# Kernel tuning notes

Measured on AMD Instinct MI355X. Metric: run time of the kernel, lower is better.

The kernel has to match this reference:

```python
import jax, jax.numpy as jnp
import numpy as np

N, E, G = 30000, 240000, 1500
EMB, NODE_DIM, EDGE_DIM, TASKS = 300, 9, 3, 12
L_ENC, L_RAT = 5, 2
GAMMA, T_CON = 0.4, 0.2


def _w(key, shape, fan_in):
    return jax.random.normal(key, shape, jnp.float32) / np.float32(np.sqrt(fan_in))


def setup_inputs() -> dict:
    key = jax.random.key(0)
    ks = jax.random.split(key, 32)
    inp = {}
    inp['x'] = jax.random.normal(ks[0], (N, NODE_DIM), jnp.float32)
    inp['edge_attr'] = jax.random.normal(ks[1], (E, EDGE_DIM), jnp.float32)
    inp['edge_index'] = jax.random.randint(ks[2], (2, E), 0, N, jnp.int32)
    b = jnp.sort(jax.random.randint(ks[3], (N,), 0, G, jnp.int32))
    inp['batch'] = b.at[0].set(0).at[-1].set(G - 1)
    u = jax.random.uniform(ks[4], (N, 2), jnp.float32, 1e-6, 1.0 - 1e-6)
    inp['gumbel'] = -jnp.log(-jnp.log(u))  # standard Gumbel noise (tau=1)
    inp['perm'] = jax.random.permutation(ks[5], G).astype(jnp.int32)
    inp['W_enc'] = _w(ks[6], (NODE_DIM, EMB), NODE_DIM)
    inp['b_enc'] = jnp.zeros((EMB,), jnp.float32)
    inp['We_g'] = _w(ks[7], (L_ENC, EDGE_DIM, EMB), EDGE_DIM)
    inp['be_g'] = jnp.zeros((L_ENC, EMB), jnp.float32)
    inp['W1_g'] = _w(ks[8], (L_ENC, EMB, 2 * EMB), EMB)
    inp['b1_g'] = jnp.zeros((L_ENC, 2 * EMB), jnp.float32)
    inp['W2_g'] = _w(ks[9], (L_ENC, 2 * EMB, EMB), 2 * EMB)
    inp['b2_g'] = jnp.zeros((L_ENC, EMB), jnp.float32)
    inp['We_r'] = _w(ks[10], (L_RAT, EDGE_DIM, EMB), EDGE_DIM)
    inp['be_r'] = jnp.zeros((L_RAT, EMB), jnp.float32)
    inp['W1_r'] = _w(ks[11], (L_RAT, EMB, 2 * EMB), EMB)
    inp['b1_r'] = jnp.zeros((L_RAT, 2 * EMB), jnp.float32)
    inp['W2_r'] = _w(ks[12], (L_RAT, 2 * EMB, EMB), 2 * EMB)
    inp['b2_r'] = jnp.zeros((L_RAT, EMB), jnp.float32)
    inp['Wg1'] = _w(ks[13], (EMB, 2 * EMB), EMB)
    inp['bg1'] = jnp.zeros((2 * EMB,), jnp.float32)
    inp['Wg2'] = _w(ks[14], (2 * EMB, 2), 2 * EMB)
    inp['bg2'] = jnp.zeros((2,), jnp.float32)
    inp['Wp1'] = _w(ks[15], (EMB, 2 * EMB), EMB)
    inp['bp1'] = jnp.zeros((2 * EMB,), jnp.float32)
    inp['Wp2'] = _w(ks[16], (2 * EMB, TASKS), 2 * EMB)
    inp['bp2'] = jnp.zeros((TASKS,), jnp.float32)
    return inp


def _gin_stack(x, src, dst, edge_attr, We, be, W1, b1, W2, b2):
    # GIN-style message passing with edge features, residual, JK='last'.
    L = We.shape[0]
    for l in range(L):
        e = edge_attr @ We[l] + be[l]                               # [E, EMB]
        msg = jax.nn.relu(x[src] + e)                                # gather [E, EMB]
        agg = jax.ops.segment_sum(msg, dst, num_segments=x.shape[0])  # scatter [N, EMB]
        h = jax.nn.relu((agg + x) @ W1[l] + b1[l]) @ W2[l] + b2[l]
        if l < L - 1:
            h = jax.nn.relu(h)
        x = x + h  # residual
    return x


def _mlp2(h, Wa, ba, Wb, bb):
    # Linear -> (BN=identity in eval) -> ReLU -> (Dropout=identity) -> Linear
    return jax.nn.relu(h @ Wa + ba) @ Wb + bb


def _forward(x, edge_attr, gumbel, W_enc, b_enc, We_g, be_g, W1_g, b1_g, W2_g, b2_g,
             We_r, be_r, W1_r, b1_r, W2_r, b2_r, Wg1, bg1, Wg2, bg2, Wp1, bp1, Wp2, bp2,
             edge_index, batch, perm):
    src, dst = edge_index[0], edge_index[1]
    cnt = jnp.clip(jax.ops.segment_sum(jnp.ones((x.shape[0],), jnp.float32), batch, num_segments=G), 1.0)[:, None]

    def gmean(v):
        return jax.ops.segment_sum(v, batch, num_segments=G) / cnt

    x_feat = x @ W_enc + b_enc                                      # node encoder
    h_node = _gin_stack(x_feat, src, dst, edge_attr, We_g, be_g, W1_g, b1_g, W2_g, b2_g)
    x_rat = _gin_stack(x_feat, src, dst, edge_attr, We_r, be_r, W1_r, b1_r, W2_r, b2_r)

    gate_logits = _mlp2(x_rat, Wg1, bg1, Wg2, bg2)                  # [N, 2]
    gate = jax.nn.softmax(gate_logits + gumbel, axis=-1)[:, 1:2]     # gumbel-softmax (soft), keep last col

    h_r = gmean(gate * h_node)
    h_env = gmean((1.0 - gate) * h_node)
    r_num = jax.ops.segment_sum(gate, batch, num_segments=G) + 1e-8
    env_num = jax.ops.segment_sum(1.0 - gate, batch, num_segments=G) + 1e-8

    pred_rem = _mlp2(h_r, Wp1, bp1, Wp2, bp2)
    loss_reg = jnp.abs(r_num / (r_num + env_num) - GAMMA).mean()

    h_out = gmean(h_node)
    na = jnp.linalg.norm(h_r, axis=1)
    nb = jnp.linalg.norm(h_out, axis=1)
    nc = jnp.linalg.norm(h_env, axis=1)
    sim = jnp.exp((h_r @ h_out.T) / (na[:, None] * nb[None, :] + 1e-8) / T_CON)
    sim_cp = jnp.exp((h_r @ h_env.T) / (na[:, None] * nc[None, :] + 1e-8) / T_CON)
    pos = jnp.diagonal(sim)
    loss_con = -jnp.log(pos / (sim_cp.sum(axis=1) + pos)).mean()

    pred_rep = _mlp2(h_r + h_env[perm], Wp1, bp1, Wp2, bp2)
    return pred_rep, pred_rem, loss_reg, loss_con


def reference(x, edge_attr, gumbel, W_enc, b_enc, We_g, be_g, W1_g, b1_g, W2_g, b2_g,
              We_r, be_r, W1_r, b1_r, W2_r, b2_r, Wg1, bg1, Wg2, bg2, Wp1, bp1, Wp2, bp2,
              edge_index, batch, perm):
    return _forward(x, edge_attr, gumbel, W_enc, b_enc, We_g, be_g, W1_g, b1_g, W2_g, b2_g,
                    We_r, be_r, W1_r, b1_r, W2_r, b2_r, Wg1, bg1, Wg2, bg2, Wp1, bp1, Wp2, bp2,
                    edge_index, batch, perm)
```

## Files before the change

kernel.cpp:

```cpp
#include <hip/hip_runtime.h>
#include <hip/hip_bf16.h>

typedef __hip_bfloat16 bf16;
typedef __attribute__((ext_vector_type(8))) short bf16x8;
typedef __attribute__((ext_vector_type(4))) float f32x4;

#define NN 30000
#define NE 240000
#define NG 1500
#define EMB 300
#define HID 600
#define NTASK 12
#define SEM 320
#define SHID 608
#define CG 75
#define NBLK_SCAN 118

__device__ __forceinline__ float tof(bf16 v){ return __bfloat162float(v); }
__device__ __forceinline__ bf16  tob(float v){ return __float2bfloat16(v); }
__device__ __forceinline__ float b2f(unsigned short u){ return __uint_as_float(((unsigned)u)<<16); }

__global__ __launch_bounds__(256) void k_hist(const int* __restrict__ dst, int* __restrict__ deg){
    int e = blockIdx.x*256 + threadIdx.x;
    if (e < NE) atomicAdd(&deg[dst[e]], 1);
}

__global__ __launch_bounds__(256) void k_scanA(const int* __restrict__ deg, int* __restrict__ bsum){
    __shared__ int red[256];
    int b = blockIdx.x, t = threadIdx.x;
    int i = b*256 + t;
    red[t] = (i < NN) ? deg[i] : 0;
    __syncthreads();
    for (int off=128; off>0; off>>=1){ if (t<off) red[t]+=red[t+off]; __syncthreads(); }
    if (t==0) bsum[b] = red[0];
}

__global__ __launch_bounds__(128) void k_scanB(const int* __restrict__ bsum, int* __restrict__ boff){
    __shared__ int s[128];
    int t = threadIdx.x;
    int v = (t < NBLK_SCAN) ? bsum[t] : 0;
    s[t] = v;
    __syncthreads();
    for (int off=1; off<128; off<<=1){
        int add = (t>=off) ? s[t-off] : 0;
        __syncthreads();
        s[t] += add;
        __syncthreads();
    }
    if (t < NBLK_SCAN) boff[t] = s[t] - v;
}

__global__ __launch_bounds__(256) void k_scanC(const int* __restrict__ deg, const int* __restrict__ boff,
                                               int* __restrict__ indptr, int* __restrict__ cursor){
    __shared__ int s[256];
    int b = blockIdx.x, t = threadIdx.x;
    int i = b*256 + t;
    int v = (i < NN) ? deg[i] : 0;
    s[t] = v;
    __syncthreads();
    for (int off=1; off<256; off<<=1){
        int add = (t>=off) ? s[t-off] : 0;
        __syncthreads();
        s[t] += add;
        __syncthreads();
    }
    int excl = s[t] - v + boff[b];
    if (i < NN){ indptr[i] = excl; cursor[i] = excl; }
    if (i == 0) indptr[NN] = NE;
}

__global__ __launch_bounds__(256) void k_scatter(const int* __restrict__ dst, int* __restrict__ cursor,
                                                 int* __restrict__ eid){
    int e = blockIdx.x*256 + threadIdx.x;
    if (e < NE){ int p = atomicAdd(&cursor[dst[e]], 1); eid[p] = e; }
}

__global__ __launch_bounds__(256) void k_eprep(const int* __restrict__ eid, const int* __restrict__ src,
                                               const float* __restrict__ eattr, float4* __restrict__ epack){
    int k = blockIdx.x*256 + threadIdx.x;
    if (k >= NE) return;
    int e = eid[k];
    float4 p;
    p.x = __int_as_float(src[e]);
    p.y = eattr[e*3]; p.z = eattr[e*3+1]; p.w = eattr[e*3+2];
    epack[k] = p;
}

__global__ __launch_bounds__(256) void k_wprep_all(
        const float* __restrict__ W1_g, const float* __restrict__ W2_g,
        const float* __restrict__ W1_r, const float* __restrict__ W2_r,
        const float* __restrict__ Wg1,  const float* __restrict__ Wp1,
        bf16* __restrict__ wt1g, bf16* __restrict__ wt2g,
        bf16* __restrict__ wt1r, bf16* __restrict__ wt2r,
        bf16* __restrict__ wtg1, bf16* __restrict__ wtp1,
        int* __restrict__ deg, const int* __restrict__ batch, int* __restrict__ gstart){
    __shared__ float t[32][33];
    int z = blockIdx.z;
    if (z == 16){
        int i = (blockIdx.y*19 + blockIdx.x)*256 + threadIdx.x;
        if (i < NN) deg[i] = 0;
        return;
    }
    if (z == 17){
        int g = (blockIdx.y*19 + blockIdx.x)*256 + threadIdx.x;
        if (g > NG) return;
        if (g == NG){ gstart[NG] = NN; return; }
        int lo=0, hi=NN;
        while (lo<hi){ int mid=(lo+hi)>>1; if (batch[mid] < g) lo=mid+1; else hi=mid; }
        gstart[g] = lo;
        return;
    }
    const float* Ws; bf16* Wd; int K, Kp, N;
    if (z < 5)      { Ws = W1_g + (size_t)z*EMB*HID;      Wd = wt1g + (size_t)z*HID*SEM;      K=EMB; Kp=SEM;  N=HID; }
    else if (z < 10){ int l=z-5;  Ws = W2_g + (size_t)l*HID*EMB; Wd = wt2g + (size_t)l*EMB*SHID; K=HID; Kp=SHID; N=EMB; }
    else if (z < 12){ int l=z-10; Ws = W1_r + (size_t)l*EMB*HID; Wd = wt1r + (size_t)l*HID*SEM;  K=EMB; Kp=SEM;  N=HID; }
    else if (z < 14){ int l=z-12; Ws = W2_r + (size_t)l*HID*EMB; Wd = wt2r + (size_t)l*EMB*SHID; K=HID; Kp=SHID; N=EMB; }
    else if (z ==14){ Ws = Wg1; Wd = wtg1; K=EMB; Kp=SEM; N=HID; }
    else            { Ws = Wp1; Wd = wtp1; K=EMB; Kp=SEM; N=HID; }
    int n0 = blockIdx.x*32, k0 = blockIdx.y*32;
    if (n0 >= N || k0 >= Kp) return;
    int tx = threadIdx.x & 31, ty = threadIdx.x >> 5;
    #pragma unroll
    for (int i=0;i<4;i++){
        int k = k0 + ty + i*8, n = n0 + tx;
        t[ty+i*8][tx] = (k<K && n<N) ? Ws[(size_t)k*N+n] : 0.f;
    }
    __syncthreads();
    #pragma unroll
    for (int i=0;i<4;i++){
        int n = n0 + ty + i*8, k = k0 + tx;
        if (n<N && k<Kp) Wd[(size_t)n*Kp+k] = tob(t[tx][ty+i*8]);
    }
}

__global__ __launch_bounds__(256) void k_encoder(const float* __restrict__ x, const float* __restrict__ W,
                                                 const float* __restrict__ b, bf16* __restrict__ xfeat){
    int idx = blockIdx.x*256 + threadIdx.x;
    if (idx >= NN*EMB) return;
    int n = idx / EMB, c = idx - n*EMB;
    float acc = b[c];
    #pragma unroll
    for (int k=0;k<9;k++) acc += x[n*9+k] * W[k*EMB+c];
    xfeat[(size_t)n*SEM + c] = tob(acc);
}

__device__ __forceinline__ void agg4_body(const bf16* __restrict__ cur, const float* __restrict__ We,
                      const float* __restrict__ be, const float4* __restrict__ epack,
                      const int* __restrict__ indptr, bf16* __restrict__ apx, int idx){
    int n = idx / CG, cg = idx - n*CG;
    int c0 = cg*4;
    float w0[4], w1[4], w2[4], bbv[4], acc[4];
    #pragma unroll
    for (int j=0;j<4;j++){
        w0[j] = We[c0+j]; w1[j] = We[EMB+c0+j]; w2[j] = We[2*EMB+c0+j]; bbv[j] = be[c0+j];
    }
    ushort4 hs = *(const ushort4*)&cur[(size_t)n*SEM + c0];
    acc[0]=b2f(hs.x); acc[1]=b2f(hs.y); acc[2]=b2f(hs.z); acc[3]=b2f(hs.w);
    int k  = indptr[n], k1 = indptr[n+1];

    auto accum4 = [&](float4 e0, float4 e1, float4 e2, float4 e3,
                      ushort4 ha, ushort4 hb, ushort4 hc, ushort4 hd){
        float fa[4] = {b2f(ha.x), b2f(ha.y), b2f(ha.z), b2f(ha.w)};
        float fb[4] = {b2f(hb.x), b2f(hb.y), b2f(hb.z), b2f(hb.w)};
        float fc[4] = {b2f(hc.x), b2f(hc.y), b2f(hc.z), b2f(hc.w)};
        float fd[4] = {b2f(hd.x), b2f(hd.y), b2f(hd.z), b2f(hd.w)};
        #pragma unroll
        for (int j=0;j<4;j++){
            float va = fa[j] + e0.y*w0[j] + e0.z*w1[j] + e0.w*w2[j] + bbv[j];
            float vb = fb[j] + e1.y*w0[j] + e1.z*w1[j] + e1.w*w2[j] + bbv[j];
            float vc = fc[j] + e2.y*w0[j] + e2.z*w1[j] + e2.w*w2[j] + bbv[j];
            float vd = fd[j] + e3.y*w0[j] + e3.z*w1[j] + e3.w*w2[j] + bbv[j];
            acc[j] += fmaxf(va, 0.f) + fmaxf(vb, 0.f) + fmaxf(vc, 0.f) + fmaxf(vd, 0.f);
        }
    };

    if (k + 4 <= k1){
        float4 e0 = epack[k], e1 = epack[k+1], e2 = epack[k+2], e3 = epack[k+3];
        ushort4 h0 = *(const ushort4*)&cur[(size_t)__float_as_int(e0.x)*SEM + c0];
        ushort4 h1 = *(const ushort4*)&cur[(size_t)__float_as_int(e1.x)*SEM + c0];
        ushort4 h2 = *(const ushort4*)&cur[(size_t)__float_as_int(e2.x)*SEM + c0];
        ushort4 h3 = *(const ushort4*)&cur[(size_t)__float_as_int(e3.x)*SEM + c0];
        while (k + 8 <= k1){
            float4 f0 = epack[k+4], f1 = epack[k+5], f2 = epack[k+6], f3 = epack[k+7];
            ushort4 g0 = *(const ushort4*)&cur[(size_t)__float_as_int(f0.x)*SEM + c0];
            ushort4 g1 = *(const ushort4*)&cur[(size_t)__float_as_int(f1.x)*SEM + c0];
            ushort4 g2 = *(const ushort4*)&cur[(size_t)__float_as_int(f2.x)*SEM + c0];
            ushort4 g3 = *(const ushort4*)&cur[(size_t)__float_as_int(f3.x)*SEM + c0];
            accum4(e0,e1,e2,e3, h0,h1,h2,h3);
            e0=f0; e1=f1; e2=f2; e3=f3;
            h0=g0; h1=g1; h2=g2; h3=g3;
            k += 4;
        }
        accum4(e0,e1,e2,e3, h0,h1,h2,h3);
        k += 4;
    }
    for (; k < k1; k++){
        float4 e0 = epack[k];
        int s0 = __float_as_int(e0.x);
        ushort4 ha = *(const ushort4*)&cur[(size_t)s0*SEM + c0];
        float fa[4] = {b2f(ha.x), b2f(ha.y), b2f(ha.z), b2f(ha.w)};
        #pragma unroll
        for (int j=0;j<4;j++){
            float va = fa[j] + e0.y*w0[j] + e0.z*w1[j] + e0.w*w2[j] + bbv[j];
            acc[j] += fmaxf(va, 0.f);
        }
    }
    ushort4 o;
    o.x = __bfloat16_as_ushort(tob(acc[0]));
    o.y = __bfloat16_as_ushort(tob(acc[1]));
    o.z = __bfloat16_as_ushort(tob(acc[2]));
    o.w = __bfloat16_as_ushort(tob(acc[3]));
    *(ushort4*)&apx[(size_t)n*SEM + c0] = o;
}

__global__ __launch_bounds__(256) void k_agg4(const bf16* __restrict__ cur, const float* __restrict__ We,
                      const float* __restrict__ be, const float4* __restrict__ epack,
                      const int* __restrict__ indptr, bf16* __restrict__ apx){
    int idx = blockIdx.x*256 + threadIdx.x;
    if (idx >= NN*CG) return;
    agg4_body(cur, We, be, epack, indptr, apx, idx);
}

__global__ __launch_bounds__(256) void k_agg4z(const bf16* __restrict__ cur0, const bf16* __restrict__ cur1,
                      const float* __restrict__ We0, const float* __restrict__ We1,
                      const float* __restrict__ be0, const float* __restrict__ be1,
                      const float4* __restrict__ epack, const int* __restrict__ indptr,
                      bf16* __restrict__ apx0, bf16* __restrict__ apx1){
    int idx = blockIdx.x*256 + threadIdx.x;
    if (idx >= NN*CG) return;
    if (blockIdx.z == 0) agg4_body(cur0, We0, be0, epack, indptr, apx0, idx);
    else                 agg4_body(cur1, We1, be1, epack, indptr, apx1, idx);
}

__global__ __launch_bounds__(256) void k_agg4d(const bf16* __restrict__ cur,
                      const float* __restrict__ WeA, const float* __restrict__ beA,
                      const float* __restrict__ WeB, const float* __restrict__ beB,
                      const float4* __restrict__ epack, const int* __restrict__ indptr,
                      bf16* __restrict__ apxA, bf16* __restrict__ apxB){
    int idx = blockIdx.x*256 + threadIdx.x;
    if (idx >= NN*CG) return;
    int n = idx / CG, cg = idx - n*CG;
    int c0 = cg*4;
    float a0[4], a1[4], a2[4], ab[4], accA[4];
    float b0[4], b1[4], b2[4], bb[4], accB[4];
    #pragma unroll
    for (int j=0;j<4;j++){
        a0[j]=WeA[c0+j]; a1[j]=WeA[EMB+c0+j]; a2[j]=WeA[2*EMB+c0+j]; ab[j]=beA[c0+j];
        b0[j]=WeB[c0+j]; b1[j]=WeB[EMB+c0+j]; b2[j]=WeB[2*EMB+c0+j]; bb[j]=beB[c0+j];
    }
    ushort4 hs = *(const ushort4*)&cur[(size_t)n*SEM + c0];
    float fs[4] = {b2f(hs.x), b2f(hs.y), b2f(hs.z), b2f(hs.w)};
    #pragma unroll
    for (int j=0;j<4;j++){ accA[j]=fs[j]; accB[j]=fs[j]; }
    int k = indptr[n], k1 = indptr[n+1];
    for (; k+2 <= k1; k += 2){
        float4 e0 = epack[k], e1 = epack[k+1];
        int s0 = __float_as_int(e0.x), s1 = __float_as_int(e1.x);
        ushort4 ha = *(const ushort4*)&cur[(size_t)s0*SEM + c0];
        ushort4 hb = *(const ushort4*)&cur[(size_t)s1*SEM + c0];
        float fa[4] = {b2f(ha.x), b2f(ha.y), b2f(ha.z), b2f(ha.w)};
        float fb[4] = {b2f(hb.x), b2f(hb.y), b2f(hb.z), b2f(hb.w)};
        #pragma unroll
        for (int j=0;j<4;j++){
            accA[j] += fmaxf(fa[j] + e0.y*a0[j] + e0.z*a1[j] + e0.w*a2[j] + ab[j], 0.f)
                     + fmaxf(fb[j] + e1.y*a0[j] + e1.z*a1[j] + e1.w*a2[j] + ab[j], 0.f);
            accB[j] += fmaxf(fa[j] + e0.y*b0[j] + e0.z*b1[j] + e0.w*b2[j] + bb[j], 0.f)
                     + fmaxf(fb[j] + e1.y*b0[j] + e1.z*b1[j] + e1.w*b2[j] + bb[j], 0.f);
        }
    }
    if (k < k1){
        float4 e0 = epack[k];
        int s0 = __float_as_int(e0.x);
        ushort4 ha = *(const ushort4*)&cur[(size_t)s0*SEM + c0];
        float fa[4] = {b2f(ha.x), b2f(ha.y), b2f(ha.z), b2f(ha.w)};
        #pragma unroll
        for (int j=0;j<4;j++){
            accA[j] += fmaxf(fa[j] + e0.y*a0[j] + e0.z*a1[j] + e0.w*a2[j] + ab[j], 0.f);
            accB[j] += fmaxf(fa[j] + e0.y*b0[j] + e0.z*b1[j] + e0.w*b2[j] + bb[j], 0.f);
        }
    }
    ushort4 oA, oB;
    oA.x=__bfloat16_as_ushort(tob(accA[0])); oA.y=__bfloat16_as_ushort(tob(accA[1]));
    oA.z=__bfloat16_as_ushort(tob(accA[2])); oA.w=__bfloat16_as_ushort(tob(accA[3]));
    oB.x=__bfloat16_as_ushort(tob(accB[0])); oB.y=__bfloat16_as_ushort(tob(accB[1]));
    oB.z=__bfloat16_as_ushort(tob(accB[2])); oB.w=__bfloat16_as_ushort(tob(accB[3]));
    *(ushort4*)&apxA[(size_t)n*SEM + c0] = oA;
    *(ushort4*)&apxB[(size_t)n*SEM + c0] = oB;
}

__device__ __forceinline__ void gemm_body(const bf16* __restrict__ A, const bf16* __restrict__ Bt,
        const float* __restrict__ bias, const bf16* __restrict__ R, bf16* __restrict__ C,
        int M, int N, int Kp, int ldc, int relu_out, short* lds){
    short* Ct = lds;
    const int CS = 136;
    int tid = threadIdx.x;
    int wave = tid >> 6, lane = tid & 63;
    int wm = wave >> 1, wn = wave & 1;
    int m0 = blockIdx.y*128, n0 = blockIdx.x*128;

    int srow = tid >> 1;
    int sq   = (tid & 1) * 2;
    int grA = min(m0 + srow, M-1);
    int grB = min(n0 + srow, N-1);
    const bf16* pA = A  + (size_t)grA*Kp + sq*8;
    const bf16* pB = Bt + (size_t)grB*Kp + sq*8;
    int aoff0 = ((srow>>4)*64 +  sq   *16 + (srow&15))*8;
    int aoff1 = ((srow>>4)*64 + (sq+1)*16 + (srow&15))*8;

    f32x4 acc[4][4];
    #pragma unroll
    for (int i=0;i<4;i++){
        #pragma unroll
        for (int j=0;j<4;j++) acc[i][j] = (f32x4){0.f,0.f,0.f,0.f};
    }

    int KC = Kp >> 5;
    uint4 ra0 = *(const uint4*)(pA);
    uint4 ra1 = *(const uint4*)(pA + 8);
    uint4 rb0 = *(const uint4*)(pB);
    uint4 rb1 = *(const uint4*)(pB + 8);
    *(uint4*)(lds + aoff0)        = ra0;
    *(uint4*)(lds + aoff1)        = ra1;
    *(uint4*)(lds + 4096 + aoff0) = rb0;
    *(uint4*)(lds + 4096 + aoff1) = rb1;
    __syncthreads();
    if (KC > 1){
        ra0 = *(const uint4*)(pA + 32); ra1 = *(const uint4*)(pA + 40);
        rb0 = *(const uint4*)(pB + 32); rb1 = *(const uint4*)(pB + 40);
    }

    for (int kc=0; kc<KC; ++kc){
        short* cbuf = lds + (kc & 1)*8192;
        short* nbuf = lds + ((kc+1) & 1)*8192;
        if (kc+1 < KC){
            *(uint4*)(nbuf + aoff0)        = ra0;
            *(uint4*)(nbuf + aoff1)        = ra1;
            *(uint4*)(nbuf + 4096 + aoff0) = rb0;
            *(uint4*)(nbuf + 4096 + aoff1) = rb1;
            if (kc+2 < KC){
                const bf16* qA = pA + (kc+2)*32;
                const bf16* qB = pB + (kc+2)*32;
                ra0 = *(const uint4*)(qA); ra1 = *(const uint4*)(qA+8);
                rb0 = *(const uint4*)(qB); rb1 = *(const uint4*)(qB+8);
            }
        }
        bf16x8 af[4], bfr[4];
        #pragma unroll
        for (int i=0;i<4;i++) af[i]  = *(const bf16x8*)(cbuf + ((wm*4+i)*64 + lane)*8);
        #pragma unroll
        for (int j=0;j<4;j++) bfr[j] = *(const bf16x8*)(cbuf + 4096 + ((wn*4+j)*64 + lane)*8);
        #pragma unroll
        for (int i=0;i<4;i++){
            #pragma unroll
            for (int j=0;j<4;j++)
                acc[i][j] = __builtin_amdgcn_mfma_f32_16x16x32_bf16(af[i], bfr[j], acc[i][j], 0, 0, 0);
        }
        __syncthreads();
    }

    int lq = lane >> 4, lr = lane & 15;
    #pragma unroll
    for (int i=0;i<4;i++){
        int rl = (wm*4+i)*16 + lq*4;
        #pragma unroll
        for (int j=0;j<4;j++){
            int cl = (wn*4+j)*16 + lr;
            float bv = bias[min(n0+cl, N-1)];
            #pragma unroll
            for (int r=0;r<4;r++){
                float v = acc[i][j][r] + bv;
                if (relu_out) v = fmaxf(v, 0.f);
                Ct[(rl+r)*CS + cl] = (short)__bfloat16_as_ushort(tob(v));
            }
        }
    }
    __syncthreads();
    #pragma unroll
    for (int p=0;p<8;p++){
        int rl = p*16 + (tid>>4);
        int cl = (tid&15)*8;
        int row = m0 + rl, col = n0 + cl;
        if (row < M && col < N){
            union { short s8[8]; uint4 v; } u;
            u.v = *(uint4*)&Ct[rl*CS + cl];
            if (R){
                const bf16* rp = &R[(size_t)row*ldc + col];
                #pragma unroll
                for (int e=0;e<8;e++){
                    float v = b2f((unsigned short)u.s8[e]) + tof(rp[e]);
                    u.s8[e] = (short)__bfloat16_as_ushort(tob(v));
                }
            }
            *(uint4*)&C[(size_t)row*ldc + col] = u.v;
        }
    }
}

__global__ __launch_bounds__(256) void k_gemm2(const bf16* __restrict__ A, const bf16* __restrict__ Bt,
        const float* __restrict__ bias, const bf16* __restrict__ R, bf16* __restrict__ C,
        int M, int N, int Kp, int ldc, int relu_out){
    __shared__ __align__(16) char ldsbuf[34816];
    gemm_body(A, Bt, bias, R, C, M, N, Kp, ldc, relu_out, (short*)ldsbuf);
}

__global__ __launch_bounds__(256) void k_gemm2z(
        const bf16* __restrict__ A0, const bf16* __restrict__ A1,
        const bf16* __restrict__ Bt0, const bf16* __restrict__ Bt1,
        const float* __restrict__ bias0, const float* __restrict__ bias1,
        const bf16* __restrict__ R0, const bf16* __restrict__ R1,
        bf16* __restrict__ C0, bf16* __restrict__ C1,
        int M, int N, int Kp, int ldc, int relu0, int relu1){
    __shared__ __align__(16) char ldsbuf[34816];
    if (blockIdx.z == 0) gemm_body(A0, Bt0, bias0, R0, C0, M, N, Kp, ldc, relu0, (short*)ldsbuf);
    else                 gemm_body(A1, Bt1, bias1, R1, C1, M, N, Kp, ldc, relu1, (short*)ldsbuf);
}

__device__ __forceinline__ void stage_tile(const short* __restrict__ P, int RB, int K, int r0, int k0,
                                           short (*lds)[64][8], int tid){
    #pragma unroll
    for (int s=0;s<2;s++){
        int seg = tid*2+s;
        int row = seg>>2, q = seg&3;
        int gr = r0 + row;
        int gk = k0 + q*8;
        union { short s8[8]; uint4 v; } u;
        if (gr < RB && gk + 8 <= K){
            const uint2* p = (const uint2*)(P + (size_t)gr*K + gk);
            uint2 lo = p[0], hi = p[1];
            u.v.x = lo.x; u.v.y = lo.y; u.v.z = hi.x; u.v.w = hi.y;
        } else {
            #pragma unroll
            for (int j=0;j<8;j++){
                int kk = gk + j;
                u.s8[j] = (gr < RB && kk < K) ? P[(size_t)gr*K + kk] : (short)0;
            }
        }
        *(uint4*)&lds[row>>4][q*16 + (row&15)][0] = u.v;
    }
}

__device__ __forceinline__ void sim_body(const bf16* __restrict__ A, const bf16* __restrict__ Bt,
                      const float* __restrict__ na, const float* __restrict__ nc, float* __restrict__ C,
                      char* ldsraw){
    short (*Asl)[64][8] = (short(*)[64][8])ldsraw;
    short (*Bsl)[64][8] = (short(*)[64][8])(ldsraw + 8192);
    int tid = threadIdx.x;
    int wave = tid >> 6, lane = tid & 63;
    int wm = wave >> 1, wn = wave & 1;
    int m0 = blockIdx.y*128, n0 = blockIdx.x*128;
    f32x4 acc[4][4];
    #pragma unroll
    for (int i=0;i<4;i++){
        #pragma unroll
        for (int j=0;j<4;j++) acc[i][j] = (f32x4){0.f,0.f,0.f,0.f};
    }
    for (int k0=0; k0<SEM; k0+=32){
        stage_tile((const short*)A,  NG, SEM, m0, k0, Asl, tid);
        stage_tile((const short*)Bt, NG, SEM, n0, k0, Bsl, tid);
        __syncthreads();
        bf16x8 af[4], bfr[4];
        #pragma unroll
        for (int i=0;i<4;i++) af[i]  = *(const bf16x8*)&Asl[wm*4+i][lane][0];
        #pragma unroll
        for (int j=0;j<4;j++) bfr[j] = *(const bf16x8*)&Bsl[wn*4+j][lane][0];
        #pragma unroll
        for (int i=0;i<4;i++){
            #pragma unroll
            for (int j=0;j<4;j++)
                acc[i][j] = __builtin_amdgcn_mfma_f32_16x16x32_bf16(af[i], bfr[j], acc[i][j], 0, 0, 0);
        }
        __syncthreads();
    }
    int lq = lane >> 4, lr = lane & 15;
    #pragma unroll
    for (int i=0;i<4;i++){
        int rb = m0 + (wm*4+i)*16 + lq*4;
        #pragma unroll
        for (int j=0;j<4;j++){
            int col = n0 + (wn*4+j)*16 + lr;
            if (col >= NG) continue;
            float ncj = nc[col];
            #pragma unroll
            for (int r=0;r<4;r++){
                int row = rb + r;
                if (row >= NG) continue;
                C[(size_t)row*NG+col] = expf(acc[i][j][r] * 5.0f / (na[row]*ncj + 1e-8f));
            }
        }
    }
}

__global__ __launch_bounds__(256) void k_simhead(const bf16* __restrict__ hrb, const bf16* __restrict__ henvb,
        const float* __restrict__ na, const float* __restrict__ nc, float* __restrict__ simcp,
        const bf16* __restrict__ Pbuf, const bf16* __restrict__ wtp1, const float* __restrict__ bp1,
        bf16* __restrict__ hidP){
    __shared__ __align__(16) char ldsbuf[34816];
    if (blockIdx.z == 0){
        if (blockIdx.x >= 12 || blockIdx.y >= 12) return;
        sim_body(hrb, henvb, na, nc, simcp, ldsbuf);
    } else {
        if (blockIdx.x >= 5) return;
        gemm_body(Pbuf, wtp1, bp1, nullptr, hidP, 2*NG, HID, SEM, SHID, 1, (short*)ldsbuf);
    }
}

__global__ __launch_bounds__(256) void k_gate(const bf16* __restrict__ mid, const float* __restrict__ Wg2,
                      const float* __restrict__ bg2, const float* __restrict__ gumbel, float* __restrict__ gate){
    int gw = blockIdx.x*4 + (threadIdx.x >> 6);
    int lane = threadIdx.x & 63;
    if (gw >= NN) return;
    float s0=0.f, s1=0.f;
    for (int i=lane;i<HID;i+=64){
        float h = tof(mid[(size_t)gw*SHID+i]);
        s0 += h * Wg2[i*2];
        s1 += h * Wg2[i*2+1];
    }
    for (int off=32; off>0; off>>=1){ s0 += __shfl_down(s0, off); s1 += __shfl_down(s1, off); }
    if (lane==0){
        float l0 = s0 + bg2[0] + gumbel[gw*2];
        float l1 = s1 + bg2[1] + gumbel[gw*2+1];
        float m = fmaxf(l0,l1);
        float e0 = expf(l0-m), e1 = expf(l1-m);
        gate[gw] = e1/(e0+e1);
    }
}

__global__ __launch_bounds__(320) void k_pool(const bf16* __restrict__ h, const float* __restrict__ gate,
                      const int* __restrict__ gstart, float* __restrict__ sumh, float* __restrict__ sumgh,
                      float* __restrict__ rnum, float* __restrict__ cntf){
    int g = blockIdx.x, c = threadIdx.x;
    if (c >= EMB) return;
    int n0 = gstart[g], n1 = gstart[g+1];
    float sh=0.f, sg=0.f, sgate=0.f;
    for (int n=n0;n<n1;n++){
        float v = tof(h[(size_t)n*SEM+c]);
        float gt = gate[n];
        sh += v; sg += gt*v;
        if (c==0) sgate += gt;
    }
    sumh[g*EMB+c] = sh; sumgh[g*EMB+c] = sg;
    if (c==0){ rnum[g] = sgate; cntf[g] = (float)(n1-n0); }
}

__global__ __launch_bounds__(320) void k_meannorm(const float* __restrict__ sumh, const float* __restrict__ sumgh,
                      const float* __restrict__ cntf, float* __restrict__ hr, float* __restrict__ henv,
                      float* __restrict__ hout, bf16* __restrict__ hrb, bf16* __restrict__ henvb,
                      bf16* __restrict__ P, float* __restrict__ na, float* __restrict__ nc,
                      float* __restrict__ pos){
    int g = blockIdx.x, c = threadIdx.x;
    float r=0.f, e=0.f, o=0.f;
    int idx = g*SEM + c;
    if (c < EMB){
        int off = g*EMB + c;
        float inv = 1.f / fmaxf(cntf[g], 1.f);
        float sh = sumh[off], sg = sumgh[off];
        r = sg*inv; e = (sh-sg)*inv; o = sh*inv;
        hr[off] = r; henv[off] = e; hout[off] = o;
        hrb[idx] = tob(r); henvb[idx] = tob(e); P[idx] = tob(r);
    } else {
        hrb[idx] = tob(0.f); henvb[idx] = tob(0.f); P[idx] = tob(0.f);
    }
    float srr=r*r, soo=o*o, see=e*e, sro=r*o;
    #pragma unroll
    for (int off=32; off>0; off>>=1){
        srr += __shfl_down(srr,off); soo += __shfl_down(soo,off);
        see += __shfl_down(see,off); sro += __shfl_down(sro,off);
    }
    __shared__ float ws[4][5];
    int wv = c >> 6, ln = c & 63;
    if (ln == 0){ ws[0][wv]=srr; ws[1][wv]=soo; ws[2][wv]=see; ws[3][wv]=sro; }
    __syncthreads();
    if (c == 0){
        float a=0.f,b=0.f,c2=0.f,d=0.f;
        #pragma unroll
        for (int i=0;i<5;i++){ a+=ws[0][i]; b+=ws[1][i]; c2+=ws[2][i]; d+=ws[3][i]; }
        float sa = sqrtf(a), sb = sqrtf(b), sc = sqrtf(c2);
        na[g] = sa; nc[g] = sc;
        pos[g] = expf(d/(sa*sb + 1e-8f) * 5.0f);
    }
}

__global__ __launch_bounds__(256) void k_pbuild2(const float* __restrict__ hr, const float* __restrict__ henv,
                      const int* __restrict__ perm, bf16* __restrict__ P){
    int idx = blockIdx.x*256 + threadIdx.x;
    if (idx >= NG*SEM) return;
    int g = idx / SEM, c = idx - g*SEM;
    P[(size_t)(NG+g)*SEM + c] = (c < EMB)
        ? tob(hr[g*EMB+c] + henv[(size_t)perm[g]*EMB + c])
        : tob(0.f);
}

__global__ __launch_bounds__(256) void k_rowsum(const float* __restrict__ simcp, float* __restrict__ S){
    __shared__ float red[256];
    int g = blockIdx.x, t = threadIdx.x;
    float s = 0.f;
    for (int j=t;j<NG;j+=256) s += simcp[(size_t)g*NG+j];
    red[t]=s; __syncthreads();
    for (int off=128; off>0; off>>=1){ if (t<off) red[t]+=red[t+off]; __syncthreads(); }
    if (t==0) S[g]=red[0];
}

__global__ __launch_bounds__(256) void k_pred(const bf16* __restrict__ hidP, const float* __restrict__ Wp2,
                      const float* __restrict__ bp2, float* __restrict__ out){
    int r = blockIdx.x*4 + (threadIdx.x >> 6);
    int lane = threadIdx.x & 63;
    if (r >= 2*NG) return;
    float acc[NTASK];
    #pragma unroll
    for (int t=0;t<NTASK;t++) acc[t] = 0.f;
    for (int i=lane;i<HID;i+=64){
        float h = tof(hidP[(size_t)r*SHID+i]);
        const float4* wp = (const float4*)&Wp2[i*NTASK];
        float4 wa = wp[0], wb = wp[1], wc = wp[2];
        acc[0]+=h*wa.x; acc[1]+=h*wa.y; acc[2]+=h*wa.z; acc[3]+=h*wa.w;
        acc[4]+=h*wb.x; acc[5]+=h*wb.y; acc[6]+=h*wb.z; acc[7]+=h*wb.w;
        acc[8]+=h*wc.x; acc[9]+=h*wc.y; acc[10]+=h*wc.z; acc[11]+=h*wc.w;
    }
    #pragma unroll
    for (int t=0;t<NTASK;t++){
        for (int off=32; off>0; off>>=1) acc[t] += __shfl_down(acc[t], off);
    }
    if (lane==0){
        float* dst = (r < NG) ? &out[NG*NTASK + r*NTASK] : &out[(r-NG)*NTASK];
        #pragma unroll
        for (int t=0;t<NTASK;t++) dst[t] = acc[t] + bp2[t];
    }
}

__global__ __launch_bounds__(256) void k_loss(const float* __restrict__ cntf, const float* __restrict__ rnum,
                      const float* __restrict__ pos, const float* __restrict__ S, float* __restrict__ out){
    __shared__ float ra[256], rb[256];
    int t = threadIdx.x;
    float a=0.f, b=0.f;
    for (int g=t; g<NG; g+=256){
        float r = rnum[g] + 1e-8f;
        float e = (cntf[g] - rnum[g]) + 1e-8f;
        a += fabsf(r/(r+e) - 0.4f);
        float p = pos[g];
        b += -logf(p/(S[g]+p));
    }
    ra[t]=a; rb[t]=b; __syncthreads();
    for (int off=128; off>0; off>>=1){ if (t<off){ ra[t]+=ra[t+off]; rb[t]+=rb[t+off]; } __syncthreads(); }
    if (t==0){
        out[2*NG*NTASK]   = ra[0]/NG;
        out[2*NG*NTASK+1] = rb[0]/NG;
    }
}

extern "C" void kernel_launch(void* const* d_in, const int* in_sizes, int n_in,
                              void* d_out, int out_size, void* d_ws, size_t ws_size,
                              hipStream_t stream) {
    const float* x      = (const float*)d_in[0];
    const float* eattr  = (const float*)d_in[1];
    const int*   eidx   = (const int*)d_in[2];
    const int*   batch  = (const int*)d_in[3];
    const float* gumbel = (const float*)d_in[4];
    const int*   perm   = (const int*)d_in[5];
    const float* W_enc  = (const float*)d_in[6];
    const float* b_enc  = (const float*)d_in[7];
    const float* We_g   = (const float*)d_in[8];
    const float* be_g   = (const float*)d_in[9];
    const float* W1_g   = (const float*)d_in[10];
    const float* b1_g   = (const float*)d_in[11];
    const float* W2_g   = (const float*)d_in[12];
    const float* b2_g   = (const float*)d_in[13];
    const float* We_r   = (const float*)d_in[14];
    const float* be_r   = (const float*)d_in[15];
    const float* W1_r   = (const float*)d_in[16];
    const float* b1_r   = (const float*)d_in[17];
    const float* W2_r   = (const float*)d_in[18];
    const float* b2_r   = (const float*)d_in[19];
    const float* Wg1    = (const float*)d_in[20];
    const float* bg1    = (const float*)d_in[21];
    const float* Wg2    = (const float*)d_in[22];
    const float* bg2    = (const float*)d_in[23];
    const float* Wp1    = (const float*)d_in[24];
    const float* bp1    = (const float*)d_in[25];
    const float* Wp2    = (const float*)d_in[26];
    const float* bp2    = (const float*)d_in[27];
    float* out = (float*)d_out;

    const int* srcArr = eidx;
    const int* dstArr = eidx + NE;

    char* w = (char*)d_ws;
    size_t off = 0;
    auto alloc = [&](size_t bytes)->char*{ char* p = w + off; off += (bytes + 255) & ~(size_t)255; return p; };
    bf16* xfeat = (bf16*)alloc((size_t)NN*SEM*2);
    bf16* cur_r = (bf16*)alloc((size_t)NN*SEM*2);
    bf16* cur_g = (bf16*)alloc((size_t)NN*SEM*2);
    bf16* apx   = (bf16*)alloc((size_t)NN*SEM*2);
    bf16* apx2  = (bf16*)alloc((size_t)NN*SEM*2);
    char* midc  = alloc((size_t)NN*SHID*2);
    bf16* mid_r = (bf16*)midc;
    float* simcp = (float*)midc;
    bf16* Pbuf   = (bf16*)(midc + 12*1024*1024);
    bf16* hidP   = (bf16*)(midc + 20*1024*1024);
    bf16* mid_g = (bf16*)alloc((size_t)NN*SHID*2);
    bf16* wt1g  = (bf16*)alloc((size_t)5*HID*SEM*2);
    bf16* wt2g  = (bf16*)alloc((size_t)5*EMB*SHID*2);
    bf16* wt1r  = (bf16*)alloc((size_t)2*HID*SEM*2);
    bf16* wt2r  = (bf16*)alloc((size_t)2*EMB*SHID*2);
    bf16* wtg1  = (bf16*)alloc((size_t)HID*SEM*2);
    bf16* wtp1  = (bf16*)alloc((size_t)HID*SEM*2);
    float4* epack = (float4*)alloc((size_t)NE*16);
    float* gate  = (float*)alloc((size_t)NN*4);
    float* sumh  = (float*)alloc((size_t)NG*EMB*4);
    float* sumgh = (float*)alloc((size_t)NG*EMB*4);
    float* hr    = (float*)alloc((size_t)NG*EMB*4);
    float* henv  = (float*)alloc((size_t)NG*EMB*4);
    float* hout  = (float*)alloc((size_t)NG*EMB*4);
    bf16* hrb    = (bf16*)alloc((size_t)NG*SEM*2);
    bf16* henvb  = (bf16*)alloc((size_t)NG*SEM*2);
    float* rnum  = (float*)alloc(NG*4);
    float* cntf  = (float*)alloc(NG*4);
    float* na    = (float*)alloc(NG*4);
    float* ncv   = (float*)alloc(NG*4);
    float* pos   = (float*)alloc(NG*4);
    float* Ssum  = (float*)alloc(NG*4);
    int* deg     = (int*)alloc((size_t)NN*4);
    int* indptr  = (int*)alloc((size_t)(NN+1)*4);
    int* cursor  = (int*)alloc((size_t)NN*4);
    int* eid     = (int*)alloc((size_t)NE*4);
    int* gstart  = (int*)alloc((size_t)(NG+1)*4);
    int* bsum    = (int*)alloc((size_t)NBLK_SCAN*4);
    int* boff    = (int*)alloc((size_t)NBLK_SCAN*4);

    const int NB_NE  = (NE+255)/256;
    const int NB_NC  = (NN*EMB+255)/256;
    const int NB_AG  = (NN*CG+255)/256;
    const int NB_GP  = (NG*SEM+255)/256;

    dim3 gwp(19, 19, 18);
    k_wprep_all<<<gwp, 256, 0, stream>>>(W1_g, W2_g, W1_r, W2_r, Wg1, Wp1,
                                         wt1g, wt2g, wt1r, wt2r, wtg1, wtp1,
                                         deg, batch, gstart);

    k_hist   <<<NB_NE, 256, 0, stream>>>(dstArr, deg);
    k_scanA  <<<NBLK_SCAN, 256, 0, stream>>>(deg, bsum);
    k_scanB  <<<1, 128, 0, stream>>>(bsum, boff);
    k_scanC  <<<NBLK_SCAN, 256, 0, stream>>>(deg, boff, indptr, cursor);
    k_scatter<<<NB_NE, 256, 0, stream>>>(dstArr, cursor, eid);
    k_eprep  <<<NB_NE, 256, 0, stream>>>(eid, srcArr, eattr, epack);

    dim3 gm1z((HID+127)/128, (NN+127)/128, 2);
    dim3 gm2z((EMB+127)/128, (NN+127)/128, 2);
    dim3 gm1((HID+127)/128, (NN+127)/128);
    dim3 gm2((EMB+127)/128, (NN+127)/128);
    dim3 gagz(NB_AG, 1, 2);

    k_encoder<<<NB_NC, 256, 0, stream>>>(x, W_enc, b_enc, xfeat);

    k_agg4d<<<NB_AG, 256, 0, stream>>>(xfeat, We_r, be_r, We_g, be_g, epack, indptr, apx, apx2);
    k_gemm2z<<<gm1z, 256, 0, stream>>>(apx, apx2, wt1r, wt1g, b1_r, b1_g,
                                       nullptr, nullptr, mid_r, mid_g, NN, HID, SEM, SHID, 1, 1);
    k_gemm2z<<<gm2z, 256, 0, stream>>>(mid_r, mid_g, wt2r, wt2g, b2_r, b2_g,
                                       xfeat, xfeat, cur_r, cur_g, NN, EMB, SHID, SEM, 1, 1);

    k_agg4z<<<gagz, 256, 0, stream>>>(cur_r, cur_g, We_r + 3*EMB, We_g + 3*EMB, be_r + EMB, be_g + EMB,
                                      epack, indptr, apx, apx2);
    k_gemm2z<<<gm1z, 256, 0, stream>>>(apx, apx2, wt1r + (size_t)HID*SEM, wt1g + (size_t)HID*SEM,
                                       b1_r + HID, b1_g + HID, nullptr, nullptr, mid_r, mid_g,
                                       NN, HID, SEM, SHID, 1, 1);
    k_gemm2z<<<gm2z, 256, 0, stream>>>(mid_r, mid_g, wt2r + (size_t)EMB*SHID, wt2g + (size_t)EMB*SHID,
                                       b2_r + EMB, b2_g + EMB, cur_r, cur_g, cur_r, cur_g,
                                       NN, EMB, SHID, SEM, 0, 1);

    k_agg4 <<<NB_AG, 256, 0, stream>>>(cur_g, We_g + 2*3*EMB, be_g + 2*EMB, epack, indptr, apx2);
    k_gemm2z<<<gm1z, 256, 0, stream>>>(cur_r, apx2, wtg1, wt1g + (size_t)2*HID*SEM,
                                       bg1, b1_g + 2*HID, nullptr, nullptr, mid_r, mid_g,
                                       NN, HID, SEM, SHID, 1, 1);
    k_gemm2<<<gm2, 256, 0, stream>>>(mid_g, wt2g + (size_t)2*EMB*SHID, b2_g + 2*EMB, cur_g, cur_g,
                                     NN, EMB, SHID, SEM, 1);
    k_gate<<<NN/4, 256, 0, stream>>>(mid_r, Wg2, bg2, gumbel, gate);

    for (int l=3; l<5; l++){
        k_agg4 <<<NB_AG, 256, 0, stream>>>(cur_g, We_g + l*3*EMB, be_g + l*EMB, epack, indptr, apx2);
        k_gemm2<<<gm1, 256, 0, stream>>>(apx2, wt1g + (size_t)l*HID*SEM, b1_g + l*HID, nullptr, mid_g,
                                         NN, HID, SEM, SHID, 1);
        k_gemm2<<<gm2, 256, 0, stream>>>(mid_g, wt2g + (size_t)l*EMB*SHID, b2_g + l*EMB, cur_g, cur_g,
                                         NN, EMB, SHID, SEM, (l<4)?1:0);
    }

    k_pool    <<<NG, 320, 0, stream>>>(cur_g, gate, gstart, sumh, sumgh, rnum, cntf);
    k_meannorm<<<NG, 320, 0, stream>>>(sumh, sumgh, cntf, hr, henv, hout, hrb, henvb, Pbuf, na, ncv, pos);
    k_pbuild2 <<<NB_GP, 256, 0, stream>>>(hr, henv, perm, Pbuf);
    dim3 gsh(12, 24, 2);
    k_simhead<<<gsh, 256, 0, stream>>>(hrb, henvb, na, ncv, simcp, Pbuf, wtp1, bp1, hidP);
    k_rowsum<<<NG, 256, 0, stream>>>(simcp, Ssum);
    k_pred  <<<(2*NG+3)/4, 256, 0, stream>>>(hidP, Wp2, bp2, out);
    k_loss  <<<1, 256, 0, stream>>>(cntf, rnum, pos, Ssum, out);
}
```

Baseline: 963.0 us.

## Co-schedule aggregation and GEMM blocks across layers in merged launches

Row ranges are split into halves so that edge aggregation for one half runs in the same launch as the MLP GEMM for the other half, and the r/g branch layers are interleaved so independent GEMMs share launches. The node encoder is folded into the weight-prep kernel as extra grid slices. The aim is to overlap the memory-bound gather/aggregate with the compute-bound matrix multiplies and fill idle CUs at stage boundaries. In exchange the schedule now depends on exact row-split constants and on mixed block types in one grid, and the number of launches in the per-layer loop goes up.

Measured after the change: 1.121 ms. 16.4% more time.

```diff
diff --git a/kernel.cpp b/kernel.cpp
--- a/kernel.cpp
+++ b/kernel.cpp
@@ -15,6 +15,19 @@
 #define SHID 608
 #define CG 75
 #define NBLK_SCAN 118
+
+#define MS 15104
+#define AGFULL_BLK 8790
+#define AGLO_BLK 4425
+#define AGHI_BLK 4365
+#define NBY_LO 118
+#define NBY_HI 117
+#define NG1_FULL 1175
+#define NG2_FULL 705
+#define NG1_LO 590
+#define NG1_HI 585
+#define NG2_LO 354
+#define NG2_HI 351
 
 __device__ __forceinline__ float tof(bf16 v){ return __bfloat162float(v); }
 __device__ __forceinline__ bf16  tob(float v){ return __float2bfloat16(v); }
@@ -93,9 +106,21 @@
         bf16* __restrict__ wt1g, bf16* __restrict__ wt2g,
         bf16* __restrict__ wt1r, bf16* __restrict__ wt2r,
         bf16* __restrict__ wtg1, bf16* __restrict__ wtp1,
-        int* __restrict__ deg, const int* __restrict__ batch, int* __restrict__ gstart){
+        int* __restrict__ deg, const int* __restrict__ batch, int* __restrict__ gstart,
+        const float* __restrict__ x, const float* __restrict__ W_enc,
+        const float* __restrict__ b_enc, bf16* __restrict__ xfeat){
     __shared__ float t[32][33];
     int z = blockIdx.z;
+    if (z >= 18){
+        int idx = ((z-18)*361 + blockIdx.y*19 + blockIdx.x)*256 + threadIdx.x;
+        if (idx >= NN*EMB) return;
+        int n = idx / EMB, c = idx - n*EMB;
+        float acc = b_enc[c];
+        #pragma unroll
+        for (int k=0;k<9;k++) acc += x[n*9+k] * W_enc[k*EMB+c];
+        xfeat[(size_t)n*SEM + c] = tob(acc);
+        return;
+    }
     if (z == 16){
         int i = (blockIdx.y*19 + blockIdx.x)*256 + threadIdx.x;
         if (i < NN) deg[i] = 0;
@@ -131,17 +156,6 @@
         int n = n0 + ty + i*8, k = k0 + tx;
         if (n<N && k<Kp) Wd[(size_t)n*Kp+k] = tob(t[tx][ty+i*8]);
     }
-}
-
-__global__ __launch_bounds__(256) void k_encoder(const float* __restrict__ x, const float* __restrict__ W,
-                                                 const float* __restrict__ b, bf16* __restrict__ xfeat){
-    int idx = blockIdx.x*256 + threadIdx.x;
-    if (idx >= NN*EMB) return;
-    int n = idx / EMB, c = idx - n*EMB;
-    float acc = b[c];
-    #pragma unroll
-    for (int k=0;k<9;k++) acc += x[n*9+k] * W[k*EMB+c];
-    xfeat[(size_t)n*SEM + c] = tob(acc);
 }
 
 __device__ __forceinline__ void agg4_body(const bf16* __restrict__ cur, const float* __restrict__ We,
@@ -215,21 +229,10 @@
 
 __global__ __launch_bounds__(256) void k_agg4(const bf16* __restrict__ cur, const float* __restrict__ We,
                       const float* __restrict__ be, const float4* __restrict__ epack,
-                      const int* __restrict__ indptr, bf16* __restrict__ apx){
-    int idx = blockIdx.x*256 + threadIdx.x;
-    if (idx >= NN*CG) return;
+                      const int* __restrict__ indptr, bf16* __restrict__ apx, int idxBase, int idxEnd){
+    int idx = idxBase + blockIdx.x*256 + threadIdx.x;
+    if (idx >= idxEnd) return;
     agg4_body(cur, We, be, epack, indptr, apx, idx);
-}
-
-__global__ __launch_bounds__(256) void k_agg4z(const bf16* __restrict__ cur0, const bf16* __restrict__ cur1,
-                      const float* __restrict__ We0, const float* __restrict__ We1,
-                      const float* __restrict__ be0, const float* __restrict__ be1,
-                      const float4* __restrict__ epack, const int* __restrict__ indptr,
-                      bf16* __restrict__ apx0, bf16* __restrict__ apx1){
-    int idx = blockIdx.x*256 + threadIdx.x;
-    if (idx >= NN*CG) return;
-    if (blockIdx.z == 0) agg4_body(cur0, We0, be0, epack, indptr, apx0, idx);
-    else                 agg4_body(cur1, We1, be1, epack, indptr, apx1, idx);
 }
 
 __global__ __launch_bounds__(256) void k_agg4d(const bf16* __restrict__ cur,
@@ -290,13 +293,12 @@
 
 __device__ __forceinline__ void gemm_body(const bf16* __restrict__ A, const bf16* __restrict__ Bt,
         const float* __restrict__ bias, const bf16* __restrict__ R, bf16* __restrict__ C,
-        int M, int N, int Kp, int ldc, int relu_out, short* lds){
+        int M, int N, int Kp, int ldc, int relu_out, short* lds, int m0, int n0){
     short* Ct = lds;
     const int CS = 136;
     int tid = threadIdx.x;
     int wave = tid >> 6, lane = tid & 63;
     int wm = wave >> 1, wn = wave & 1;
-    int m0 = blockIdx.y*128, n0 = blockIdx.x*128;
 
     int srow = tid >> 1;
     int sq   = (tid & 1) * 2;
@@ -398,9 +400,10 @@
 
 __global__ __launch_bounds__(256) void k_gemm2(const bf16* __restrict__ A, const bf16* __restrict__ Bt,
         const float* __restrict__ bias, const bf16* __restrict__ R, bf16* __restrict__ C,
-        int M, int N, int Kp, int ldc, int relu_out){
+        int M, int N, int Kp, int ldc, int relu_out, int mBase){
     __shared__ __align__(16) char ldsbuf[34816];
-    gemm_body(A, Bt, bias, R, C, M, N, Kp, ldc, relu_out, (short*)ldsbuf);
+    gemm_body(A, Bt, bias, R, C, M, N, Kp, ldc, relu_out, (short*)ldsbuf,
+              mBase + blockIdx.y*128, blockIdx.x*128);
 }
 
 __global__ __launch_bounds__(256) void k_gemm2z(
@@ -411,8 +414,49 @@
         bf16* __restrict__ C0, bf16* __restrict__ C1,
         int M, int N, int Kp, int ldc, int relu0, int relu1){
     __shared__ __align__(16) char ldsbuf[34816];
-    if (blockIdx.z == 0) gemm_body(A0, Bt0, bias0, R0, C0, M, N, Kp, ldc, relu0, (short*)ldsbuf);
-    else                 gemm_body(A1, Bt1, bias1, R1, C1, M, N, Kp, ldc, relu1, (short*)ldsbuf);
+    int m0 = blockIdx.y*128, n0 = blockIdx.x*128;
+    if (blockIdx.z == 0) gemm_body(A0, Bt0, bias0, R0, C0, M, N, Kp, ldc, relu0, (short*)ldsbuf, m0, n0);
+    else                 gemm_body(A1, Bt1, bias1, R1, C1, M, N, Kp, ldc, relu1, (short*)ldsbuf, m0, n0);
+}
+
+__global__ __launch_bounds__(256) void k_gemm2d(
+        const bf16* __restrict__ A0, const bf16* __restrict__ Bt0, const float* __restrict__ b0,
+        const bf16* __restrict__ R0, bf16* __restrict__ C0,
+        int M0, int N0, int K0, int ldc0, int relu0, int mBase0, int nbx0, int ng0,
+        const bf16* __restrict__ A1, const bf16* __restrict__ Bt1, const float* __restrict__ b1,
+        const bf16* __restrict__ R1, bf16* __restrict__ C1,
+        int M1, int N1, int K1, int ldc1, int relu1, int mBase1, int nbx1){
+    __shared__ __align__(16) char ldsbuf[34816];
+    int bid = blockIdx.x;
+    if (bid < ng0){
+        gemm_body(A0, Bt0, b0, R0, C0, M0, N0, K0, ldc0, relu0, (short*)ldsbuf,
+                  mBase0 + (bid/nbx0)*128, (bid%nbx0)*128);
+    } else {
+        int gb = bid - ng0;
+        gemm_body(A1, Bt1, b1, R1, C1, M1, N1, K1, ldc1, relu1, (short*)ldsbuf,
+                  mBase1 + (gb/nbx1)*128, (gb%nbx1)*128);
+    }
+}
+
+__global__ __launch_bounds__(256) void k_aggemm(
+        const bf16* __restrict__ cur, const float* __restrict__ We, const float* __restrict__ be,
+        const float4* __restrict__ epack, const int* __restrict__ indptr, bf16* __restrict__ apx,
+        int aggIdxBase, int aggIdxEnd, int na,
+        const bf16* __restrict__ A, const bf16* __restrict__ Bt, const float* __restrict__ bias,
+        const bf16* __restrict__ R, bf16* __restrict__ C,
+        int M, int N, int Kp, int ldc, int relu, int mBase, int nbx, int ng){
+    __shared__ __align__(16) char ldsbuf[34816];
+    int bid = blockIdx.x;
+    int T = na + ng;
+    int fb  = (int)(((long long)bid * ng) / T);
+    int fb1 = (int)(((long long)(bid+1) * ng) / T);
+    if (fb1 > fb){
+        gemm_body(A, Bt, bias, R, C, M, N, Kp, ldc, relu, (short*)ldsbuf,
+                  mBase + (fb/nbx)*128, (fb%nbx)*128);
+    } else {
+        int idx = aggIdxBase + (bid - fb)*256 + threadIdx.x;
+        if (idx < aggIdxEnd) agg4_body(cur, We, be, epack, indptr, apx, idx);
+    }
 }
 
 __device__ __forceinline__ void stage_tile(const short* __restrict__ P, int RB, int K, int r0, int k0,
@@ -500,7 +544,8 @@
         sim_body(hrb, henvb, na, nc, simcp, ldsbuf);
     } else {
         if (blockIdx.x >= 5) return;
-        gemm_body(Pbuf, wtp1, bp1, nullptr, hidP, 2*NG, HID, SEM, SHID, 1, (short*)ldsbuf);
+        gemm_body(Pbuf, wtp1, bp1, nullptr, hidP, 2*NG, HID, SEM, SHID, 1, (short*)ldsbuf,
+                  blockIdx.y*128, blockIdx.x*128);
     }
 }
 
@@ -727,14 +772,13 @@
     int* boff    = (int*)alloc((size_t)NBLK_SCAN*4);
 
     const int NB_NE  = (NE+255)/256;
-    const int NB_NC  = (NN*EMB+255)/256;
     const int NB_AG  = (NN*CG+255)/256;
     const int NB_GP  = (NG*SEM+255)/256;
 
-    dim3 gwp(19, 19, 18);
+    dim3 gwp(19, 19, 18 + 98);
     k_wprep_all<<<gwp, 256, 0, stream>>>(W1_g, W2_g, W1_r, W2_r, Wg1, Wp1,
                                          wt1g, wt2g, wt1r, wt2r, wtg1, wtp1,
-                                         deg, batch, gstart);
+                                         deg, batch, gstart, x, W_enc, b_enc, xfeat);
 
     k_hist   <<<NB_NE, 256, 0, stream>>>(dstArr, deg);
     k_scanA  <<<NBLK_SCAN, 256, 0, stream>>>(deg, bsum);
@@ -744,42 +788,42 @@
     k_eprep  <<<NB_NE, 256, 0, stream>>>(eid, srcArr, eattr, epack);
 
     dim3 gm1z((HID+127)/128, (NN+127)/128, 2);
-    dim3 gm2z((EMB+127)/128, (NN+127)/128, 2);
-    dim3 gm1((HID+127)/128, (NN+127)/128);
-    dim3 gm2((EMB+127)/128, (NN+127)/128);
-    dim3 gagz(NB_AG, 1, 2);
-
-    k_encoder<<<NB_NC, 256, 0, stream>>>(x, W_enc, b_enc, xfeat);
 
     k_agg4d<<<NB_AG, 256, 0, stream>>>(xfeat, We_r, be_r, We_g, be_g, epack, indptr, apx, apx2);
     k_gemm2z<<<gm1z, 256, 0, stream>>>(apx, apx2, wt1r, wt1g, b1_r, b1_g,
                                        nullptr, nullptr, mid_r, mid_g, NN, HID, SEM, SHID, 1, 1);
-    k_gemm2z<<<gm2z, 256, 0, stream>>>(mid_r, mid_g, wt2r, wt2g, b2_r, b2_g,
-                                       xfeat, xfeat, cur_r, cur_g, NN, EMB, SHID, SEM, 1, 1);
-
-    k_agg4z<<<gagz, 256, 0, stream>>>(cur_r, cur_g, We_r + 3*EMB, We_g + 3*EMB, be_r + EMB, be_g + EMB,
-                                      epack, indptr, apx, apx2);
-    k_gemm2z<<<gm1z, 256, 0, stream>>>(apx, apx2, wt1r + (size_t)HID*SEM, wt1g + (size_t)HID*SEM,
-                                       b1_r + HID, b1_g + HID, nullptr, nullptr, mid_r, mid_g,
-                                       NN, HID, SEM, SHID, 1, 1);
-    k_gemm2z<<<gm2z, 256, 0, stream>>>(mid_r, mid_g, wt2r + (size_t)EMB*SHID, wt2g + (size_t)EMB*SHID,
-                                       b2_r + EMB, b2_g + EMB, cur_r, cur_g, cur_r, cur_g,
-                                       NN, EMB, SHID, SEM, 0, 1);
-
-    k_agg4 <<<NB_AG, 256, 0, stream>>>(cur_g, We_g + 2*3*EMB, be_g + 2*EMB, epack, indptr, apx2);
-    k_gemm2z<<<gm1z, 256, 0, stream>>>(cur_r, apx2, wtg1, wt1g + (size_t)2*HID*SEM,
-                                       bg1, b1_g + 2*HID, nullptr, nullptr, mid_r, mid_g,
-                                       NN, HID, SEM, SHID, 1, 1);
-    k_gemm2<<<gm2, 256, 0, stream>>>(mid_g, wt2g + (size_t)2*EMB*SHID, b2_g + 2*EMB, cur_g, cur_g,
-                                     NN, EMB, SHID, SEM, 1);
+    k_gemm2<<<dim3(3,235), 256, 0, stream>>>(mid_r, wt2r, b2_r, xfeat, cur_r, NN, EMB, SHID, SEM, 1, 0);
+    k_aggemm<<<AGFULL_BLK + NG2_FULL, 256, 0, stream>>>(
+        cur_r, We_r + 3*EMB, be_r + EMB, epack, indptr, apx, 0, NN*CG, AGFULL_BLK,
+        mid_g, wt2g, b2_g, xfeat, cur_g, NN, EMB, SHID, SEM, 1, 0, 3, NG2_FULL);
+    k_aggemm<<<AGFULL_BLK + NG1_FULL, 256, 0, stream>>>(
+        cur_g, We_g + 3*EMB, be_g + EMB, epack, indptr, apx2, 0, NN*CG, AGFULL_BLK,
+        apx, wt1r + (size_t)HID*SEM, b1_r + HID, nullptr, mid_r, NN, HID, SEM, SHID, 1, 0, 5, NG1_FULL);
+    k_gemm2d<<<NG2_FULL + NG1_FULL, 256, 0, stream>>>(
+        mid_r, wt2r + (size_t)EMB*SHID, b2_r + EMB, cur_r, cur_r, NN, EMB, SHID, SEM, 0, 0, 3, NG2_FULL,
+        apx2, wt1g + (size_t)HID*SEM, b1_g + HID, nullptr, mid_g, NN, HID, SEM, SHID, 1, 0, 5);
+    k_gemm2d<<<NG1_FULL + NG2_FULL, 256, 0, stream>>>(
+        cur_r, wtg1, bg1, nullptr, mid_r, NN, HID, SEM, SHID, 1, 0, 5, NG1_FULL,
+        mid_g, wt2g + (size_t)EMB*SHID, b2_g + EMB, cur_g, cur_g, NN, EMB, SHID, SEM, 1, 0, 3);
     k_gate<<<NN/4, 256, 0, stream>>>(mid_r, Wg2, bg2, gumbel, gate);
 
-    for (int l=3; l<5; l++){
-        k_agg4 <<<NB_AG, 256, 0, stream>>>(cur_g, We_g + l*3*EMB, be_g + l*EMB, epack, indptr, apx2);
-        k_gemm2<<<gm1, 256, 0, stream>>>(apx2, wt1g + (size_t)l*HID*SEM, b1_g + l*HID, nullptr, mid_g,
-                                         NN, HID, SEM, SHID, 1);
-        k_gemm2<<<gm2, 256, 0, stream>>>(mid_g, wt2g + (size_t)l*EMB*SHID, b2_g + l*EMB, cur_g, cur_g,
-                                         NN, EMB, SHID, SEM, (l<4)?1:0);
+    for (int l=2; l<5; l++){
+        const float* We = We_g + l*3*EMB;
+        const float* be = be_g + l*EMB;
+        const bf16* w1 = wt1g + (size_t)l*HID*SEM;
+        const float* b1 = b1_g + l*HID;
+        const bf16* w2 = wt2g + (size_t)l*EMB*SHID;
+        const float* b2 = b2_g + l*EMB;
+        int relu2 = (l<4) ? 1 : 0;
+        k_agg4<<<AGLO_BLK, 256, 0, stream>>>(cur_g, We, be, epack, indptr, apx2, 0, MS*CG);
+        k_aggemm<<<AGHI_BLK + NG1_LO, 256, 0, stream>>>(
+            cur_g, We, be, epack, indptr, apx2, MS*CG, NN*CG, AGHI_BLK,
+            apx2, w1, b1, nullptr, mid_g, NN, HID, SEM, SHID, 1, 0, 5, NG1_LO);
+        k_gemm2d<<<NG1_HI + NG2_LO, 256, 0, stream>>>(
+            apx2, w1, b1, nullptr, mid_g, NN, HID, SEM, SHID, 1, MS, 5, NG1_HI,
+            mid_g, w2, b2, cur_g, cur_g, NN, EMB, SHID, SEM, relu2, 0, 3);
+        k_gemm2<<<dim3(3, NBY_HI), 256, 0, stream>>>(mid_g, w2, b2, cur_g, cur_g,
+                                                     NN, EMB, SHID, SEM, relu2, MS);
     }
 
     k_pool    <<<NG, 320, 0, stream>>>(cur_g, gate, gstart, sumh, sumgh, rnum, cntf);
```
